# Kernel tuning notes

Hardware: AMD Instinct MI355X
Metric: run time of the kernel (lower is better)

## Reference

```python
import jax, jax.numpy as jnp
import numpy as np

NG = 6      # K*2 graphs
N = 6000    # nodes per graph
E = 96000   # edges per graph
F_IN = 128  # input node feature dim
C = 128     # ggnn_args['out_channels']
BINS = 21


def setup_inputs() -> dict:
    key = jax.random.key(0)
    ks = jax.random.split(key, 5)
    x = jax.random.normal(ks[0], (NG, N, F_IN), jnp.float32)
    edge_index = jax.random.randint(ks[1], (NG, 2, E), 0, N, dtype=jnp.int64)
    edge_attr = jax.random.uniform(ks[2], (NG, E, 6), dtype=jnp.float32)
    # 4 GCNConv layers: Linear (no bias inside lin) + separate bias param
    gcn_W = jax.random.normal(ks[3], (4, F_IN, C), jnp.float32) / np.sqrt(F_IN)
    gcn_b = jnp.zeros((4, C), jnp.float32)
    # 4 xavier-init Ws matrices
    Ws = jax.random.normal(ks[4], (4, C, C), jnp.float32) / np.sqrt(C)
    return {"x": x, "edge_index": edge_index, "edge_attr": edge_attr,
            "gcn_W": gcn_W, "gcn_b": gcn_b, "Ws": Ws}


def _gcn(x, row, col, w, W, b):
    """PyG GCNConv with edge weights: add self-loops (weight 1), symmetric norm."""
    n = x.shape[0]
    loop = jnp.arange(n)
    r = jnp.concatenate([row, loop])
    c = jnp.concatenate([col, loop])
    ww = jnp.concatenate([w, jnp.ones((n,), w.dtype)])
    deg = jax.ops.segment_sum(ww, c, num_segments=n)
    dis = jnp.where(deg > 0, jax.lax.rsqrt(jnp.maximum(deg, 1e-30)), 0.0)
    norm = dis[r] * ww * dis[c]
    h = x @ W  # [n, C]
    out = jax.ops.segment_sum(norm[:, None] * h[r], c, num_segments=n)
    return out + b


def _gnn_layer(x, ei, ea, gcn_W, gcn_b, Ws):
    row, col = ei[0], ei[1]
    acc = jnp.zeros((x.shape[0], C), x.dtype)
    for i in range(4):  # fixed small structural loop
        h = jax.nn.relu(_gcn(x, row, col, ea[:, i + 2], gcn_W[i], gcn_b[i]))
        acc = acc + h @ Ws[i]
    return acc


def reference(x, edge_index, edge_attr, gcn_W, gcn_b, Ws):
    # per-graph GNN features [NG, N, C]
    feats = jax.vmap(lambda xi, ei, ea: _gnn_layer(xi, ei, ea, gcn_W, gcn_b, Ws))(
        x, edge_index, edge_attr)
    # g_matrix: concat of per-graph mean embeddings -> [1, NG*C]
    g_matrix = feats.mean(axis=1).reshape(1, NG * C)
    # L2-normalize rows (F.normalize, eps=1e-12)
    nrm = jnp.linalg.norm(feats, axis=-1, keepdims=True)
    xn = feats / jnp.maximum(nrm, 1e-12)
    centers = jnp.linspace(-1.0, 1.0, BINS, dtype=jnp.float32)  # -1.0 .. 1.0 step 0.1
    width = 2.0 / BINS  # histc bin width over [-1, 1]
    rows = []
    for i1 in range(NG):
        vals = []
        for i2 in range(NG):
            t = jnp.tanh(xn[i1] @ xn[i2].T)  # [N, N]
            idx = jnp.clip(jnp.floor((t + 1.0) / width), 0, BINS - 1).astype(jnp.int32)
            hist = jnp.bincount(idx.ravel(), length=BINS).astype(jnp.float32)
            hist = hist / (N * N)
            vals.append(jnp.dot(hist, centers))
        rows.append(jnp.stack(vals))
    sim_matrix = jnp.stack(rows)[None]  # [1, NG, NG]
    return g_matrix, sim_matrix
```

## Files before the change

### kernel.cpp

```cpp
#include <hip/hip_runtime.h>

#define NG 6
#define NN 6000
#define NE 96000
#define NP2 6144

typedef unsigned int uint;
typedef unsigned short ushort;
typedef __attribute__((ext_vector_type(8))) short short8;
typedef __attribute__((ext_vector_type(4))) float f32x4;
typedef __attribute__((ext_vector_type(2))) float f32x2;

__device__ __forceinline__ ushort f2bf(float f){
  uint u = __float_as_uint(f);
  u = (u + 0x7fffu + ((u >> 16) & 1u)) >> 16;
  return (ushort)u;
}
__device__ __forceinline__ float bf2f(uint u){ return __uint_as_float(u << 16); }

__device__ __forceinline__ void async16(const void* g, void* l){
  __builtin_amdgcn_global_load_lds(
      (const __attribute__((address_space(1))) unsigned int*)g,
      (__attribute__((address_space(3))) unsigned int*)l, 16, 0, 0);
}

__device__ __constant__ int c_i1[21] = {0,0,0,0,0,0,1,1,1,1,1,2,2,2,2,3,3,3,4,4,5};
__device__ __constant__ int c_i2[21] = {0,1,2,3,4,5,1,2,3,4,5,2,3,4,5,3,4,5,4,5,5};
__device__ __constant__ int c_nd[15] = {1,2,3,4,5,7,8,9,10,12,13,14,16,17,19};
__device__ __constant__ int c_dg[6]  = {0,6,11,15,18,20};
__device__ __constant__ int c_dcum[25] = {0,6,12,18,24,29,34,39,44,48,52,56,60,
                                          63,66,69,72,74,76,78,80,81,82,83,84};

__device__ __forceinline__ void stage128s(const ushort* __restrict__ gsrc, int stride,
                                          ushort* lds, int w, int lane){
  #pragma unroll
  for (int i = 0; i < 8; i++){
    int off = (w*8 + i) * 512;
    int rowi = (w*8 + i)*4 + (lane >> 4);
    int chunk = (lane & 15) ^ (rowi & 15);
    async16(gsrc + (size_t)rowi*stride + chunk*8, (void*)&lds[off]);
  }
}

__device__ __forceinline__ void stage64s(const ushort* __restrict__ gsrc,
                                         ushort* lds, int w, int lane){
  #pragma unroll
  for (int i = 0; i < 4; i++){
    int off = (w*4 + i) * 512;
    int rowi = (w*4 + i)*4 + (lane >> 4);
    int chunk = (lane & 15) ^ (rowi & 15);
    async16(gsrc + (size_t)rowi*128 + chunk*8, (void*)&lds[off]);
  }
}

__device__ __forceinline__ void mfma128(const ushort* As, const ushort* Bs,
                                        int w, int lane, f32x4 acc[4][4]){
  int q = lane >> 4, cl = lane & 15;
  int wm = w >> 1, wn = w & 1;
  #pragma unroll
  for (int ks = 0; ks < 4; ks++){
    short8 af[4], bfr[4];
    int ch = ((ks*4 + q) ^ cl) * 8;
    #pragma unroll
    for (int m = 0; m < 4; m++) af[m]  = *(const short8*)&As[(wm*64 + m*16 + cl)*128 + ch];
    #pragma unroll
    for (int n = 0; n < 4; n++) bfr[n] = *(const short8*)&Bs[(wn*64 + n*16 + cl)*128 + ch];
    #pragma unroll
    for (int m = 0; m < 4; m++)
      #pragma unroll
      for (int n = 0; n < 4; n++)
        acc[m][n] = __builtin_amdgcn_mfma_f32_16x16x32_bf16(af[m], bfr[n], acc[m][n], 0, 0, 0);
  }
}
__device__ __forceinline__ void zacc(f32x4 acc[4][4]){
  #pragma unroll
  for (int m = 0; m < 4; m++)
    #pragma unroll
    for (int n = 0; n < 4; n++) acc[m][n] = (f32x4){0.f,0.f,0.f,0.f};
}

#define TC1 10.499108f
#define TC3 (-3.4888668f)
#define TC5 1.3464888f
#define TC7 (-0.4433517f)
#define TC9 0.0833385f
__device__ __forceinline__ f32x2 psumT(const f32x4 acc[4][4]){
  f32x2 t2 = {0.f, 0.f};
  #pragma unroll
  for (int m = 0; m < 4; m++)
    #pragma unroll
    for (int n = 0; n < 4; n++)
      #pragma unroll
      for (int rp = 0; rp < 2; rp++){
        f32x2 d = { acc[m][n][rp*2], acc[m][n][rp*2+1] };
        f32x2 t = d*d;
        f32x2 qq = t*TC9 + TC7;
        qq = qq*t + TC5;
        qq = qq*t + TC3;
        qq = qq*t + TC1;
        t2 = d*qq + t2;
      }
  return t2;
}

__global__ void k_zero4(float4* p, int n16){
  int i = blockIdx.x*256 + threadIdx.x;
  if (i < n16) p[i] = make_float4(0.f,0.f,0.f,0.f);
}
__global__ void k_zero1(float* p, int n){
  int i = blockIdx.x*256 + threadIdx.x;
  if (i < n) p[i] = 0.f;
}
__global__ void k_cvtx(const float4* x, uint2* xbf, int n4){
  int i = blockIdx.x*256 + threadIdx.x;
  if (i >= n4) return;
  float4 v = x[i];
  xbf[i] = make_uint2((uint)f2bf(v.x) | ((uint)f2bf(v.y) << 16),
                      (uint)f2bf(v.z) | ((uint)f2bf(v.w) << 16));
}
__global__ void k_cvt_w(const float* W, const float* Wsm, ushort* Wtc, ushort* Wstc){
  int i = blockIdx.x*256 + threadIdx.x;
  int l = i >> 14, rem = i & 16383;
  int a = rem >> 7, b = rem & 127;
  Wtc[(l << 14) + b*128 + a] = f2bf(W[i]);
  Wstc[b*512 + l*128 + a]    = f2bf(Wsm[i]);
}
__global__ void k_count(const int* ei, int* counts){
  int i = blockIdx.x*256 + threadIdx.x;
  if (i >= NG*NE) return;
  int g = i / NE, e = i - g*NE;
  atomicAdd(&counts[g*NN + ei[g*2*NE + NE + e]], 1);
}
__global__ void k_scan(const int* counts, int* offs, int* cursor){
  __shared__ int sm[256];
  int g = blockIdx.x, t = threadIdx.x;
  const int* c = counts + g*NN;
  int i0 = t*24, i1 = i0 + 24; if (i1 > NN) i1 = NN; if (i0 > NN) i0 = NN;
  int s = 0;
  for (int i = i0; i < i1; i++) s += c[i];
  sm[t] = s;
  __syncthreads();
  for (int off = 1; off < 256; off <<= 1){
    int v = (t >= off) ? sm[t - off] : 0;
    __syncthreads();
    sm[t] += v;
    __syncthreads();
  }
  int run = sm[t] - s;
  for (int i = i0; i < i1; i++){
    offs[g*NN + i] = run; cursor[g*NN + i] = run; run += c[i];
  }
}
__global__ void k_place(const int* ei, int* cursor, int2* elist2){
  int i = blockIdx.x*256 + threadIdx.x;
  if (i >= NG*NE) return;
  int g = i / NE, e = i - g*NE;
  int col = ei[g*2*NE + NE + e];
  int row = ei[g*2*NE + e];
  int pos = atomicAdd(&cursor[g*NN + col], 1);
  elist2[g*NE + pos] = make_int2(e, row);
}
__global__ void k_deg(const float* __restrict__ ea, const int* __restrict__ offs,
                      const int* __restrict__ counts, const int2* __restrict__ elist2,
                      float4* __restrict__ dis4){
  int i = blockIdx.x*256 + threadIdx.x;
  if (i >= NG*NN) return;
  int g = i / NN;
  int beg = offs[i], cnt = counts[i];
  const int2* el = elist2 + (size_t)g*NE;
  const float* eag = ea + (size_t)g*NE*6;
  float4 s = make_float4(1.f,1.f,1.f,1.f);
  for (int j = 0; j < cnt; j++){
    int e = el[beg + j].x;
    float2 wa = *(const float2*)(eag + (size_t)e*6 + 2);
    float2 wb = *(const float2*)(eag + (size_t)e*6 + 4);
    s.x += wa.x; s.y += wa.y; s.z += wb.x; s.w += wb.y;
  }
  dis4[i] = make_float4(rsqrtf(fmaxf(s.x,1e-30f)), rsqrtf(fmaxf(s.y,1e-30f)),
                        rsqrtf(fmaxf(s.z,1e-30f)), rsqrtf(fmaxf(s.w,1e-30f)));
}

__global__ __launch_bounds__(256) void k_gather1(const float* __restrict__ ea,
    const float4* __restrict__ dis4, const int* __restrict__ offs,
    const int* __restrict__ counts, const int2* __restrict__ elist2,
    const ushort* __restrict__ xbf, ushort* __restrict__ agg, int c){
  __shared__ int    sr[4][64];
  __shared__ float4 sc[4][64];
  int lane = threadIdx.x, wy = threadIdx.y;
  int nidx = blockIdx.x*4 + wy;
  int lg = nidx / NN, n = nidx - lg*NN;
  int g = c*2 + lg;
  float4 dn4 = dis4[g*NN + n];
  const uint* xrow = (const uint*)xbf + (size_t)lg*NN*64;
  uint xv = xrow[(size_t)n*64 + lane];
  f32x2 xs = {bf2f(xv & 0xffffu), bf2f(xv >> 16)};
  f32x2 a0 = xs*dn4.x, a1 = xs*dn4.y, a2 = xs*dn4.z, a3 = xs*dn4.w;
  int beg = offs[g*NN + n], cnt = counts[g*NN + n];
  const int2*  el  = elist2 + (size_t)g*NE;
  const float* eag = ea + (size_t)g*NE*6;
  for (int j0 = 0; j0 < cnt; j0 += 64){
    int take = cnt - j0; if (take > 64) take = 64;
    if (lane < take){
      int2 er = el[beg + j0 + lane];
      float2 wa = *(const float2*)(eag + (size_t)er.x*6 + 2);
      float2 wb = *(const float2*)(eag + (size_t)er.x*6 + 4);
      float4 dr = dis4[g*NN + er.y];
      sr[wy][lane] = er.y;
      sc[wy][lane] = make_float4(wa.x*dr.x, wa.y*dr.y, wb.x*dr.z, wb.y*dr.w);
    }
    int j = 0;
    for (; j + 4 <= take; j += 4){
      int r0 = sr[wy][j], r1 = sr[wy][j+1], r2 = sr[wy][j+2], r3 = sr[wy][j+3];
      float4 c0 = sc[wy][j], c1 = sc[wy][j+1], c2 = sc[wy][j+2], c3 = sc[wy][j+3];
      uint x0 = xrow[(size_t)r0*64 + lane];
      uint x1 = xrow[(size_t)r1*64 + lane];
      uint x2 = xrow[(size_t)r2*64 + lane];
      uint x3 = xrow[(size_t)r3*64 + lane];
      f32x2 v;
      v = (f32x2){bf2f(x0 & 0xffffu), bf2f(x0 >> 16)};
      a0 = v*c0.x + a0; a1 = v*c0.y + a1; a2 = v*c0.z + a2; a3 = v*c0.w + a3;
      v = (f32x2){bf2f(x1 & 0xffffu), bf2f(x1 >> 16)};
      a0 = v*c1.x + a0; a1 = v*c1.y + a1; a2 = v*c1.z + a2; a3 = v*c1.w + a3;
      v = (f32x2){bf2f(x2 & 0xffffu), bf2f(x2 >> 16)};
      a0 = v*c2.x + a0; a1 = v*c2.y + a1; a2 = v*c2.z + a2; a3 = v*c2.w + a3;
      v = (f32x2){bf2f(x3 & 0xffffu), bf2f(x3 >> 16)};
      a0 = v*c3.x + a0; a1 = v*c3.y + a1; a2 = v*c3.z + a2; a3 = v*c3.w + a3;
    }
    for (; j < take; j++){
      int r0 = sr[wy][j];
      float4 c0 = sc[wy][j];
      uint x0 = xrow[(size_t)r0*64 + lane];
      f32x2 v = (f32x2){bf2f(x0 & 0xffffu), bf2f(x0 >> 16)};
      a0 = v*c0.x + a0; a1 = v*c0.y + a1; a2 = v*c0.z + a2; a3 = v*c0.w + a3;
    }
  }
  a0 = a0*dn4.x; a1 = a1*dn4.y; a2 = a2*dn4.z; a3 = a3*dn4.w;
  uint* ag = (uint*)agg;
  ag[((size_t)((lg*4+0)*NN + n))*64 + lane] = (uint)f2bf(a0.x) | ((uint)f2bf(a0.y) << 16);
  ag[((size_t)((lg*4+1)*NN + n))*64 + lane] = (uint)f2bf(a1.x) | ((uint)f2bf(a1.y) << 16);
  ag[((size_t)((lg*4+2)*NN + n))*64 + lane] = (uint)f2bf(a2.x) | ((uint)f2bf(a2.y) << 16);
  ag[((size_t)((lg*4+3)*NN + n))*64 + lane] = (uint)f2bf(a3.x) | ((uint)f2bf(a3.y) << 16);
}

__global__ __launch_bounds__(256) void k_gemm1b(const ushort* __restrict__ agg,
    const ushort* __restrict__ Wtc, const float* __restrict__ gb,
    ushort* __restrict__ H){
  __shared__ ushort As[16384];
  __shared__ ushort Bsh[16384];
  int by = blockIdx.y;
  int lg = by >> 2, l = by & 3;
  int tid = threadIdx.x, w = tid >> 6, lane = tid & 63;
  stage128s(agg + (size_t)by*NN*128 + (size_t)blockIdx.x*16384, 128, As, w, lane);
  stage128s(Wtc + (l << 14), 128, Bsh, w, lane);
  __syncthreads();
  f32x4 acc[4][4];
  zacc(acc);
  mfma128(As, Bsh, w, lane, acc);
  int q = lane >> 4, cl = lane & 15, wm = w >> 1, wn = w & 1;
  int rowb = blockIdx.x*128 + wm*64 + q*4;
  int colb = wn*64 + cl;
  #pragma unroll
  for (int m = 0; m < 4; m++)
    #pragma unroll
    for (int n = 0; n < 4; n++)
      #pragma unroll
      for (int r = 0; r < 4; r++){
        int row = rowb + m*16 + r, col = colb + n*16;
        if (row < NN){
          float v = fmaxf(acc[m][n][r] + gb[l*128 + col], 0.f);
          H[((size_t)(lg*NN + row))*512 + l*128 + col] = f2bf(v);
        }
      }
}

__global__ __launch_bounds__(256) void k_gemm2(const ushort* __restrict__ A,
    const ushort* __restrict__ B, float* __restrict__ feats, int coff){
  __shared__ ushort As[16384];
  __shared__ ushort Bsh[16384];
  int tid = threadIdx.x, w = tid >> 6, lane = tid & 63;
  f32x4 acc[4][4];
  zacc(acc);
  #pragma unroll
  for (int kc = 0; kc < 4; kc++){
    if (kc) __syncthreads();
    stage128s(A + (size_t)blockIdx.x*128*512 + kc*128, 512, As, w, lane);
    stage128s(B + kc*128, 512, Bsh, w, lane);
    __syncthreads();
    mfma128(As, Bsh, w, lane, acc);
  }
  int q = lane >> 4, cl = lane & 15, wm = w >> 1, wn = w & 1;
  int rowb = blockIdx.x*128 + wm*64 + q*4;
  int colb = wn*64 + cl;
  #pragma unroll
  for (int m = 0; m < 4; m++)
    #pragma unroll
    for (int n = 0; n < 4; n++)
      #pragma unroll
      for (int r = 0; r < 4; r++){
        int row = rowb + m*16 + r;
        if (row < 2*NN)
          feats[(size_t)(coff + row)*128 + colb + n*16] = acc[m][n][r];
      }
}

__global__ void k_mean(const float* feats, float* out){
  int g = blockIdx.x / 48, ch = blockIdx.x - g*48;
  int c = threadIdx.x;
  float s = 0.f;
  int n0 = ch*125;
  for (int n = n0; n < n0 + 125; n++) s += feats[((size_t)(g*NN + n))*128 + c];
  atomicAdd(&out[g*128 + c], s * (1.0f/6000.0f));
}

__global__ void k_xn(const float* feats, ushort* xn){
  int lane = threadIdx.x;
  int rall = blockIdx.x*4 + threadIdx.y;
  int g = rall / NP2, rl = rall - g*NP2;
  uint* dst = (uint*)&xn[((size_t)(g*NP2 + rl))*128];
  if (rl < NN){
    const float2* src = (const float2*)&feats[((size_t)(g*NN + rl))*128];
    float2 v = src[lane];
    float ss = v.x*v.x + v.y*v.y;
    #pragma unroll
    for (int s = 32; s > 0; s >>= 1) ss += __shfl_xor(ss, s);
    float inv = 1.0f / fmaxf(sqrtf(ss), 1e-12f);
    dst[lane] = (uint)f2bf(v.x*inv) | ((uint)f2bf(v.y*inv) << 16);
  } else {
    dst[lane] = 0u;
  }
}

__global__ __launch_bounds__(256, 2) void k_pair(const ushort* __restrict__ xn,
                                                 float* Spart){
  __shared__ ushort Bs[2][8192];
  int bx = blockIdx.x;
  int p, rt, c0, niter; bool diag;
  if (bx < 2160){
    int pp = bx / 144, rem = bx - pp*144;
    rt = rem / 6; int ch = rem - rt*6;
    p = c_nd[pp]; diag = false; c0 = ch*16; niter = 16;
  } else {
    int idd = bx - 2160;
    int pd = idd / 84, rem = idd - pd*84;
    int r_ = 0;
    while (c_dcum[r_ + 1] <= rem) r_++;
    rt = r_;
    int ch = rem - c_dcum[rt];
    p = c_dg[pd]; diag = true;
    c0 = 4*rt + ch*16;
    int left = 96 - c0;
    niter = left < 16 ? left : 16;
  }
  int i1 = c_i1[p], i2 = c_i2[p];
  int tid = threadIdx.x, w = tid >> 6, lane = tid & 63;
  int q = lane >> 4, cl = lane & 15;
  const ushort* Arow = xn + ((size_t)i1*NP2 + rt*256 + w*64 + cl)*128;
  short8 afr[4][4];
  #pragma unroll
  for (int m = 0; m < 4; m++)
    #pragma unroll
    for (int ks = 0; ks < 4; ks++)
      afr[m][ks] = *(const short8*)&Arow[m*16*128 + ks*32 + q*8];
  const ushort* Bbase = xn + ((size_t)i2*NP2)*128;
  stage64s(Bbase + (size_t)c0*8192, Bs[0], w, lane);
  f32x2 totw = {0.f, 0.f};
  for (int it = 0; it < niter; it++){
    int cur = it & 1;
    __syncthreads();
    if (it + 1 < niter)
      stage64s(Bbase + (size_t)(c0+it+1)*8192, Bs[1-cur], w, lane);
    f32x4 acc[4][4];
    __builtin_amdgcn_s_setprio(1);
    {
      short8 bfr[4];
      int ch0 = (q ^ cl) * 8;
      #pragma unroll
      for (int n = 0; n < 4; n++)
        bfr[n] = *(const short8*)&Bs[cur][(n*16 + cl)*128 + ch0];
      f32x4 z4 = {0.f,0.f,0.f,0.f};
      #pragma unroll
      for (int m = 0; m < 4; m++)
        #pragma unroll
        for (int n = 0; n < 4; n++)
          acc[m][n] = __builtin_amdgcn_mfma_f32_16x16x32_bf16(afr[m][0], bfr[n], z4, 0, 0, 0);
    }
    #pragma unroll
    for (int ks = 1; ks < 4; ks++){
      short8 bfr[4];
      int ch = ((ks*4 + q) ^ cl) * 8;
      #pragma unroll
      for (int n = 0; n < 4; n++)
        bfr[n] = *(const short8*)&Bs[cur][(n*16 + cl)*128 + ch];
      #pragma unroll
      for (int m = 0; m < 4; m++)
        #pragma unroll
        for (int n = 0; n < 4; n++)
          acc[m][n] = __builtin_amdgcn_mfma_f32_16x16x32_bf16(afr[m][ks], bfr[n], acc[m][n], 0, 0, 0);
    }
    __builtin_amdgcn_s_setprio(0);
    f32x2 t2 = psumT(acc);
    float wgt = (diag && (c0 + it) >= 4*rt + 4) ? 2.f : 1.f;
    totw = t2*wgt + totw;
  }
  float tot = totw.x + totw.y;
  #pragma unroll
  for (int s = 32; s > 0; s >>= 1) tot += __shfl_xor(tot, s);
  if (lane == 0) atomicAdd(&Spart[p*64 + (bx & 63)], tot);
}

__global__ void k_final(const float* Spart, float* out){
  int t = threadIdx.x;
  if (t < 21){
    float s = 0.f;
    for (int j = 0; j < 64; j++) s += Spart[t*64 + j];
    float v = s * (1.0f/360000000.0f);
    int i1 = c_i1[t], i2 = c_i2[t];
    out[768 + i1*6 + i2] = v;
    out[768 + i2*6 + i1] = v;
  }
}

extern "C" void kernel_launch(void* const* d_in, const int* in_sizes, int n_in,
                              void* d_out, int out_size, void* d_ws, size_t ws_size,
                              hipStream_t stream){
  (void)in_sizes; (void)n_in; (void)out_size; (void)ws_size;
  const float* x   = (const float*)d_in[0];
  const int*   ei  = (const int*)d_in[1];
  const float* ea  = (const float*)d_in[2];
  const float* gW  = (const float*)d_in[3];
  const float* gb  = (const float*)d_in[4];
  const float* Wsm = (const float*)d_in[5];
  float* out = (float*)d_out;
  char* ws = (char*)d_ws;
  float*  feats  = (float*) (ws + 0);
  int*    counts = (int*)   (ws + 18432000);
  int*    offs   = (int*)   (ws + 18576000);
  int*    cursor = (int*)   (ws + 18720000);
  float*  Spart  = (float*) (ws + 18864000);
  float4* dis4   = (float4*)(ws + 18872192);
  int2*   elist2 = (int2*)  (ws + 19448192);
  ushort* Wtc    = (ushort*)(ws + 24056192);
  ushort* Wstc   = (ushort*)(ws + 24187264);
  ushort* xbf    = (ushort*)(ws + 24318336);
  ushort* agg    = (ushort*)(ws + 27394560);
  ushort* H      = (ushort*)(ws + 39690752);
  ushort* xnbf   = (ushort*)(ws + 24318336);

  k_zero4<<<dim3(108), dim3(256), 0, stream>>>((float4*)(ws + 18432000), 27512);
  k_zero1<<<dim3(4),   dim3(256), 0, stream>>>(out, 804);
  k_cvt_w<<<dim3(256), dim3(256), 0, stream>>>(gW, Wsm, Wtc, Wstc);
  k_count<<<dim3(2250), dim3(256), 0, stream>>>(ei, counts);
  k_scan <<<dim3(6),    dim3(256), 0, stream>>>(counts, offs, cursor);
  k_place<<<dim3(2250), dim3(256), 0, stream>>>(ei, cursor, elist2);
  k_deg  <<<dim3(141),  dim3(256), 0, stream>>>(ea, offs, counts, elist2, dis4);
  for (int c = 0; c < 3; c++){
    k_cvtx   <<<dim3(1500), dim3(256), 0, stream>>>(
        (const float4*)(x + (size_t)c*2*NN*128), (uint2*)xbf, 384000);
    k_gather1<<<dim3(3000), dim3(64,4), 0, stream>>>(ea, dis4, offs, counts, elist2,
                                                     xbf, agg, c);
    k_gemm1b <<<dim3(47,8), dim3(256), 0, stream>>>(agg, Wtc, gb, H);
    k_gemm2  <<<dim3(94),   dim3(256), 0, stream>>>(H, Wstc, feats, c*2*NN);
  }
  k_mean <<<dim3(288),  dim3(128),  0, stream>>>(feats, out);
  k_xn   <<<dim3(9216), dim3(64,4), 0, stream>>>(feats, xnbf);
  k_pair <<<dim3(2664), dim3(256),  0, stream>>>(xnbf, Spart);
  k_final<<<dim3(1),    dim3(64),   0, stream>>>(Spart, out);
}
```

Baseline: 535.6 us.

## Software-pipeline tanh-sum epilogue with next tile's MFMAs in similarity kernel

Splits the 64x64 per-wave accumulator into two halves and restructures the loop so the polynomial tanh reduction of the previous tile's results runs interleaved with the MFMAs of the current tile. The aim is to overlap VALU epilogue work with matrix-core work instead of running them back to back. It keeps two accumulator sets live across iterations, which adds register pressure, and the weight for each tile is now applied one iteration late.

```diff
diff --git a/kernel.cpp b/kernel.cpp
--- a/kernel.cpp
+++ b/kernel.cpp
@@ -101,6 +101,52 @@
         t2 = d*qq + t2;
       }
   return t2;
+}
+
+__device__ __forceinline__ f32x2 psum24(const f32x4 acc[4][2]){
+  f32x2 t2 = {0.f, 0.f};
+  #pragma unroll
+  for (int m = 0; m < 4; m++)
+    #pragma unroll
+    for (int n = 0; n < 2; n++)
+      #pragma unroll
+      for (int rp = 0; rp < 2; rp++){
+        f32x2 d = { acc[m][n][rp*2], acc[m][n][rp*2+1] };
+        f32x2 t = d*d;
+        f32x2 qq = t*TC9 + TC7;
+        qq = qq*t + TC5;
+        qq = qq*t + TC3;
+        qq = qq*t + TC1;
+        t2 = d*qq + t2;
+      }
+  return t2;
+}
+
+__device__ __forceinline__ void half_mfma(const ushort* __restrict__ Bsc,
+                                          const short8 afr[4][4], int q, int cl,
+                                          int nb, f32x4 acc[4][2]){
+  const f32x4 z4 = {0.f,0.f,0.f,0.f};
+  {
+    int ch0 = (q ^ cl) * 8;
+    short8 b0 = *(const short8*)&Bsc[((nb  )*16 + cl)*128 + ch0];
+    short8 b1 = *(const short8*)&Bsc[((nb+1)*16 + cl)*128 + ch0];
+    #pragma unroll
+    for (int m = 0; m < 4; m++){
+      acc[m][0] = __builtin_amdgcn_mfma_f32_16x16x32_bf16(afr[m][0], b0, z4, 0, 0, 0);
+      acc[m][1] = __builtin_amdgcn_mfma_f32_16x16x32_bf16(afr[m][0], b1, z4, 0, 0, 0);
+    }
+  }
+  #pragma unroll
+  for (int ks = 1; ks < 4; ks++){
+    int ch = ((ks*4 + q) ^ cl) * 8;
+    short8 b0 = *(const short8*)&Bsc[((nb  )*16 + cl)*128 + ch];
+    short8 b1 = *(const short8*)&Bsc[((nb+1)*16 + cl)*128 + ch];
+    #pragma unroll
+    for (int m = 0; m < 4; m++){
+      acc[m][0] = __builtin_amdgcn_mfma_f32_16x16x32_bf16(afr[m][ks], b0, acc[m][0], 0, 0, 0);
+      acc[m][1] = __builtin_amdgcn_mfma_f32_16x16x32_bf16(afr[m][ks], b1, acc[m][1], 0, 0, 0);
+    }
+  }
 }
 
 __global__ void k_zero4(float4* p, int n16){
@@ -364,43 +410,33 @@
   const ushort* Bbase = xn + ((size_t)i2*NP2)*128;
   stage64s(Bbase + (size_t)c0*8192, Bs[0], w, lane);
   f32x2 totw = {0.f, 0.f};
-  for (int it = 0; it < niter; it++){
+  f32x4 accA[4][2], accB[4][2];
+  __syncthreads();
+  if (niter > 1)
+    stage64s(Bbase + (size_t)(c0+1)*8192, Bs[1], w, lane);
+  __builtin_amdgcn_s_setprio(1);
+  half_mfma(Bs[0], afr, q, cl, 0, accA);
+  half_mfma(Bs[0], afr, q, cl, 2, accB);
+  __builtin_amdgcn_s_setprio(0);
+  float pw = (diag && c0 >= 4*rt + 4) ? 2.f : 1.f;
+  for (int it = 1; it < niter; it++){
     int cur = it & 1;
     __syncthreads();
     if (it + 1 < niter)
       stage64s(Bbase + (size_t)(c0+it+1)*8192, Bs[1-cur], w, lane);
-    f32x4 acc[4][4];
     __builtin_amdgcn_s_setprio(1);
-    {
-      short8 bfr[4];
-      int ch0 = (q ^ cl) * 8;
-      #pragma unroll
-      for (int n = 0; n < 4; n++)
-        bfr[n] = *(const short8*)&Bs[cur][(n*16 + cl)*128 + ch0];
-      f32x4 z4 = {0.f,0.f,0.f,0.f};
-      #pragma unroll
-      for (int m = 0; m < 4; m++)
-        #pragma unroll
-        for (int n = 0; n < 4; n++)
-          acc[m][n] = __builtin_amdgcn_mfma_f32_16x16x32_bf16(afr[m][0], bfr[n], z4, 0, 0, 0);
-    }
-    #pragma unroll
-    for (int ks = 1; ks < 4; ks++){
-      short8 bfr[4];
-      int ch = ((ks*4 + q) ^ cl) * 8;
-      #pragma unroll
-      for (int n = 0; n < 4; n++)
-        bfr[n] = *(const short8*)&Bs[cur][(n*16 + cl)*128 + ch];
-      #pragma unroll
-      for (int m = 0; m < 4; m++)
-        #pragma unroll
-        for (int n = 0; n < 4; n++)
-          acc[m][n] = __builtin_amdgcn_mfma_f32_16x16x32_bf16(afr[m][ks], bfr[n], acc[m][n], 0, 0, 0);
-    }
+    f32x2 t2a = psum24(accA);
+    half_mfma(Bs[cur], afr, q, cl, 0, accA);
+    f32x2 t2b = psum24(accB);
+    half_mfma(Bs[cur], afr, q, cl, 2, accB);
     __builtin_amdgcn_s_setprio(0);
-    f32x2 t2 = psumT(acc);
-    float wgt = (diag && (c0 + it) >= 4*rt + 4) ? 2.f : 1.f;
-    totw = t2*wgt + totw;
+    totw = (t2a + t2b)*pw + totw;
+    pw = (diag && (c0 + it) >= 4*rt + 4) ? 2.f : 1.f;
+  }
+  {
+    f32x2 t2a = psum24(accA);
+    f32x2 t2b = psum24(accB);
+    totw = (t2a + t2b)*pw + totw;
   }
   float tot = totw.x + totw.y;
   #pragma unroll
```

After: 543.0 us. No clear change (+1.4%).

## Switch pairwise similarity GEMM from bf16 to fp8 scaled MFMA

Applied to the files above, without the earlier changes.

Normalized features are now stored as fp8 (e4m3) instead of bf16, and the pairwise N×N similarity kernel uses the 16x16x128 f8f6f4 scaled MFMA, covering the whole 128-wide K in a single instruction per tile. This halves LDS staging and global traffic for the B tiles and cuts the MFMA instruction count by 4x. The cost is lower precision in the tanh-histogram inputs, which may shift bin assignments near bin edges.

```diff
diff --git a/kernel.cpp b/kernel.cpp
--- a/kernel.cpp
+++ b/kernel.cpp
@@ -7,7 +7,9 @@
 
 typedef unsigned int uint;
 typedef unsigned short ushort;
+typedef unsigned char uchar;
 typedef __attribute__((ext_vector_type(8))) short short8;
+typedef __attribute__((ext_vector_type(8))) int int8v;
 typedef __attribute__((ext_vector_type(4))) float f32x4;
 typedef __attribute__((ext_vector_type(2))) float f32x2;
 
@@ -42,14 +44,15 @@
   }
 }
 
-__device__ __forceinline__ void stage64s(const ushort* __restrict__ gsrc,
-                                         ushort* lds, int w, int lane){
-  #pragma unroll
-  for (int i = 0; i < 4; i++){
-    int off = (w*4 + i) * 512;
-    int rowi = (w*4 + i)*4 + (lane >> 4);
-    int chunk = (lane & 15) ^ (rowi & 15);
-    async16(gsrc + (size_t)rowi*128 + chunk*8, (void*)&lds[off]);
+__device__ __forceinline__ void stage8(const uchar* __restrict__ gsrc,
+                                       uchar* lds, int w, int lane){
+  #pragma unroll
+  for (int j = 0; j < 2; j++){
+    int cj = w*2 + j;
+    int d = cj*64 + lane;
+    int row = d >> 3, slot = d & 7;
+    async16(gsrc + (size_t)row*128 + ((slot ^ (row & 7)) << 4),
+            (void*)(lds + cj*1024));
   }
 }
 
@@ -312,11 +315,11 @@
   atomicAdd(&out[g*128 + c], s * (1.0f/6000.0f));
 }
 
-__global__ void k_xn(const float* feats, ushort* xn){
+__global__ void k_xn(const float* feats, uchar* xn8){
   int lane = threadIdx.x;
   int rall = blockIdx.x*4 + threadIdx.y;
   int g = rall / NP2, rl = rall - g*NP2;
-  uint* dst = (uint*)&xn[((size_t)(g*NP2 + rl))*128];
+  ushort* dst = (ushort*)(xn8 + ((size_t)(g*NP2 + rl))*128);
   if (rl < NN){
     const float2* src = (const float2*)&feats[((size_t)(g*NN + rl))*128];
     float2 v = src[lane];
@@ -324,15 +327,16 @@
     #pragma unroll
     for (int s = 32; s > 0; s >>= 1) ss += __shfl_xor(ss, s);
     float inv = 1.0f / fmaxf(sqrtf(ss), 1e-12f);
-    dst[lane] = (uint)f2bf(v.x*inv) | ((uint)f2bf(v.y*inv) << 16);
+    int pk = __builtin_amdgcn_cvt_pk_fp8_f32(v.x*inv, v.y*inv, 0, false);
+    dst[lane] = (ushort)(pk & 0xffff);
   } else {
-    dst[lane] = 0u;
-  }
-}
-
-__global__ __launch_bounds__(256, 2) void k_pair(const ushort* __restrict__ xn,
+    dst[lane] = 0;
+  }
+}
+
+__global__ __launch_bounds__(256, 2) void k_pair(const uchar* __restrict__ xn8,
                                                  float* Spart){
-  __shared__ ushort Bs[2][8192];
+  __shared__ uchar Bs[2][8192];
   int bx = blockIdx.x;
   int p, rt, c0, niter; bool diag;
   if (bx < 2160){
@@ -354,49 +358,42 @@
   int i1 = c_i1[p], i2 = c_i2[p];
   int tid = threadIdx.x, w = tid >> 6, lane = tid & 63;
   int q = lane >> 4, cl = lane & 15;
-  const ushort* Arow = xn + ((size_t)i1*NP2 + rt*256 + w*64 + cl)*128;
-  short8 afr[4][4];
-  #pragma unroll
-  for (int m = 0; m < 4; m++)
-    #pragma unroll
-    for (int ks = 0; ks < 4; ks++)
-      afr[m][ks] = *(const short8*)&Arow[m*16*128 + ks*32 + q*8];
-  const ushort* Bbase = xn + ((size_t)i2*NP2)*128;
-  stage64s(Bbase + (size_t)c0*8192, Bs[0], w, lane);
+  const uchar* Arow = xn8 + ((size_t)i1*NP2 + rt*256 + w*64 + cl)*128 + q*32;
+  int8v afr[4];
+  #pragma unroll
+  for (int m = 0; m < 4; m++){
+    uint4 lo = *(const uint4*)(Arow + m*2048);
+    uint4 hi = *(const uint4*)(Arow + m*2048 + 16);
+    afr[m] = (int8v){(int)lo.x,(int)lo.y,(int)lo.z,(int)lo.w,
+                     (int)hi.x,(int)hi.y,(int)hi.z,(int)hi.w};
+  }
+  int b0 = cl*128 + (((q*2  ) ^ (cl & 7)) << 4);
+  int b1 = cl*128 + (((q*2+1) ^ (cl & 7)) << 4);
+  const uchar* Bbase = xn8 + (size_t)i2*NP2*128;
+  stage8(Bbase + (size_t)c0*8192, Bs[0], w, lane);
   f32x2 totw = {0.f, 0.f};
+  const f32x4 z4 = {0.f,0.f,0.f,0.f};
   for (int it = 0; it < niter; it++){
     int cur = it & 1;
     __syncthreads();
     if (it + 1 < niter)
-      stage64s(Bbase + (size_t)(c0+it+1)*8192, Bs[1-cur], w, lane);
+      stage8(Bbase + (size_t)(c0+it+1)*8192, Bs[1-cur], w, lane);
+    __builtin_amdgcn_s_setprio(1);
+    int8v bfr[4];
+    #pragma unroll
+    for (int n = 0; n < 4; n++){
+      uint4 lo = *(const uint4*)&Bs[cur][b0 + n*2048];
+      uint4 hi = *(const uint4*)&Bs[cur][b1 + n*2048];
+      bfr[n] = (int8v){(int)lo.x,(int)lo.y,(int)lo.z,(int)lo.w,
+                       (int)hi.x,(int)hi.y,(int)hi.z,(int)hi.w};
+    }
     f32x4 acc[4][4];
-    __builtin_amdgcn_s_setprio(1);
-    {
-      short8 bfr[4];
-      int ch0 = (q ^ cl) * 8;
+    #pragma unroll
+    for (int m = 0; m < 4; m++)
       #pragma unroll
       for (int n = 0; n < 4; n++)
-        bfr[n] = *(const short8*)&Bs[cur][(n*16 + cl)*128 + ch0];
-      f32x4 z4 = {0.f,0.f,0.f,0.f};
-      #pragma unroll
-      for (int m = 0; m < 4; m++)
-        #pragma unroll
-        for (int n = 0; n < 4; n++)
-          acc[m][n] = __builtin_amdgcn_mfma_f32_16x16x32_bf16(afr[m][0], bfr[n], z4, 0, 0, 0);
-    }
-    #pragma unroll
-    for (int ks = 1; ks < 4; ks++){
-      short8 bfr[4];
-      int ch = ((ks*4 + q) ^ cl) * 8;
-      #pragma unroll
-      for (int n = 0; n < 4; n++)
-        bfr[n] = *(const short8*)&Bs[cur][(n*16 + cl)*128 + ch];
-      #pragma unroll
-      for (int m = 0; m < 4; m++)
-        #pragma unroll
-        for (int n = 0; n < 4; n++)
-          acc[m][n] = __builtin_amdgcn_mfma_f32_16x16x32_bf16(afr[m][ks], bfr[n], acc[m][n], 0, 0, 0);
-    }
+        acc[m][n] = __builtin_amdgcn_mfma_scale_f32_16x16x128_f8f6f4(
+            afr[m], bfr[n], z4, 0, 0, 0, 0x7F, 0, 0x7F);
     __builtin_amdgcn_s_setprio(0);
     f32x2 t2 = psumT(acc);
     float wgt = (diag && (c0 + it) >= 4*rt + 4) ? 2.f : 1.f;
@@ -444,7 +441,7 @@
   ushort* xbf    = (ushort*)(ws + 24318336);
   ushort* agg    = (ushort*)(ws + 27394560);
   ushort* H      = (ushort*)(ws + 39690752);
-  ushort* xnbf   = (ushort*)(ws + 24318336);
+  uchar*  xn8    = (uchar*) (ws + 24318336);
 
   k_zero4<<<dim3(108), dim3(256), 0, stream>>>((float4*)(ws + 18432000), 27512);
   k_zero1<<<dim3(4),   dim3(256), 0, stream>>>(out, 804);
@@ -462,7 +459,7 @@
     k_gemm2  <<<dim3(94),   dim3(256), 0, stream>>>(H, Wstc, feats, c*2*NN);
   }
   k_mean <<<dim3(288),  dim3(128),  0, stream>>>(feats, out);
-  k_xn   <<<dim3(9216), dim3(64,4), 0, stream>>>(feats, xnbf);
-  k_pair <<<dim3(2664), dim3(256),  0, stream>>>(xnbf, Spart);
+  k_xn   <<<dim3(9216), dim3(64,4), 0, stream>>>(feats, xn8);
+  k_pair <<<dim3(2664), dim3(256),  0, stream>>>(xn8, Spart);
   k_final<<<dim3(1),    dim3(64),   0, stream>>>(Spart, out);
 }
```

Result: faster. 472.2 us (-11.8%).
